# Kernel tuning notes

Hardware: AMD Instinct MI355X
Metric: run time of the kernel (lower is better)

The kernel has to match this reference:

```python
import jax, jax.numpy as jnp
import numpy as np
from functools import partial

EPS = 1e-10


@partial(jax.custom_vjp, nondiff_argnums=(1,))
def kwta(x, k):
    # k-WTA: keep top-k values along last dim, zero elsewhere (STE backward).
    vals, _ = jax.lax.top_k(x, k)
    thresh = vals[..., -1:]
    return jnp.where(x >= thresh, x, jnp.zeros((), x.dtype))


def _kwta_fwd(x, k):
    out = kwta(x, k)
    mask = (out != 0).astype(x.dtype)  # matches torch: mask = (out != 0)
    return out, mask


def _kwta_bwd(k, mask, g):
    return (g * mask,)


kwta.defvjp(_kwta_fwd, _kwta_bwd)


def _sparsify(x, W_down, k):
    h = jax.nn.relu(x @ W_down.T)          # (B, T, N_ca3)
    h = kwta(h, k)
    norm = jnp.maximum(jnp.linalg.norm(h, axis=-1, keepdims=True), EPS)
    return h / norm


def _retrieve_successor(sparse, W_ca3, k):
    # retrieval_steps = 1; replicate the early-break on all-zero activity.
    h = jax.nn.relu(sparse @ W_ca3.T)       # (B, T, N_ca3)
    valid = h.sum() >= EPS
    hk = kwta(h, k)
    norm = jnp.maximum(jnp.linalg.norm(hk, axis=-1, keepdims=True), EPS)
    return jnp.where(valid, hk / norm, sparse)


def setup_inputs() -> dict:
    key = jax.random.key(0)
    k1, k2, k3, k4, k5, k6 = jax.random.split(key, 6)
    B, T, D, N = 4, 2048, 1024, 4096
    x = jax.random.normal(k1, (B, T, D), dtype=jnp.float32)
    # xavier_normal: std = gain * sqrt(2 / (fan_in + fan_out))
    W_down = jax.random.normal(k2, (N, D), dtype=jnp.float32) * (0.5 * np.sqrt(2.0 / (D + N)))
    W_up = jax.random.normal(k3, (D, N), dtype=jnp.float32) * (0.1 * np.sqrt(2.0 / (D + N)))
    # gate_proj weight is zero-init in torch; use small random for a nontrivial gate
    W_gate = jax.random.normal(k4, (D, D), dtype=jnp.float32) * 0.02
    b_gate = jnp.full((D,), -2.0, dtype=jnp.float32)
    # W_ca3 buffer is zero-init then Hebbian-learned; random stand-in
    W_ca3 = jax.random.normal(k6, (N, N), dtype=jnp.float32) * 0.02
    return {"x": x, "W_down": W_down, "W_up": W_up, "W_gate": W_gate,
            "b_gate": b_gate, "W_ca3": W_ca3, "k": 64}


def reference(x, W_down, W_up, W_gate, b_gate, W_ca3, k):
    sparse = _sparsify(x, W_down, k)                    # (B, T, N)
    successor = _retrieve_successor(sparse, W_ca3, k)   # (B, T, N)
    prediction = successor @ W_up.T                     # (B, T, D)
    g = jax.nn.sigmoid(x @ W_gate.T + b_gate)           # (B, T, D)
    return x + g * prediction
```

## Files before the change

### kernel.cpp

```cpp
#include <hip/hip_runtime.h>
#include <hip/hip_bf16.h>
#include <stdint.h>

typedef float f32x4 __attribute__((ext_vector_type(4)));
typedef int i32x4 __attribute__((ext_vector_type(4)));

#define MROWS 8192
#define DD 1024
#define DN 4096

__device__ __forceinline__ void load_lds16(const void* g, void* l) {
  __builtin_amdgcn_global_load_lds((const __attribute__((address_space(1))) void*)g,
                                   (__attribute__((address_space(3))) void*)l, 16, 0, 0);
}

__device__ __forceinline__ unsigned f32_to_bf16_rne(float f) {
  unsigned u = __float_as_uint(f);
  return (u + 0x7fffu + ((u >> 16) & 1u)) >> 16;
}

template<int EPI>
__global__ void __launch_bounds__(512, 1)
gemm_i8_4ph(const uint8_t* __restrict__ A, const uint8_t* __restrict__ B,
            __hip_bfloat16* __restrict__ Cb, int M, int N, int K,
            float* __restrict__ vsum,
            const float* __restrict__ sA, const float* __restrict__ sB)
{
  extern __shared__ __align__(16) char smem[];
  const int tid  = threadIdx.x;
  const int lane = tid & 63;
  const int wave = tid >> 6;
  const int wm = wave >> 2;
  const int wn = wave & 3;

  const int nwg = gridDim.x;
  const int bid = ((int)blockIdx.x % 8) * (nwg >> 3) + ((int)blockIdx.x >> 3);

  const int nbn = N >> 8;
  const int bm = (bid / nbn) << 8;
  const int bn = (bid % nbn) << 8;

  const int NT = K >> 7;

  i32x4 acc[8][4];
  const i32x4 izero = {0, 0, 0, 0};
#pragma unroll
  for (int i = 0; i < 8; ++i)
#pragma unroll
    for (int j = 0; j < 4; ++j)
      acc[i][j] = izero;

  const int csb = (((tid & 3) ^ ((tid >> 3) & 3)) << 4);
  const uint8_t* Ag = A + (size_t)(bm + (tid >> 2)) * K + csb;
  const uint8_t* Bg = B + (size_t)(bn + (tid >> 2)) * K + csb;

  const int rl = lane & 15;
  const int kc = lane >> 4;
  const int chunk_off = ((kc ^ ((rl >> 1) & 3)) << 4);
  const int aoff = ((wm << 7) + rl) * 64 + chunk_off;
  const int boff = ((wn << 6) + rl) * 64 + chunk_off;

#define STAGE_AB(S, KH) do { \
    const int kt_ = (((S) & (NT - 1)) << 7) + ((KH) << 6); \
    char* da_ = smem + (((((S) & 1) << 1) | (KH)) << 14) + (tid << 4); \
    load_lds16(Ag + kt_, da_); \
    load_lds16(Ag + (size_t)128 * K + kt_, da_ + 8192); \
    load_lds16(Bg + kt_, da_ + 65536); \
    load_lds16(Bg + (size_t)128 * K + kt_, da_ + 65536 + 8192); \
  } while (0)

  i32x4 a0, a1, a2, a3, a4, a5, a6, a7, b0, b1, b2, b3;

#define MFMA_ROW8(MI, AF) \
    acc[MI][0] = __builtin_amdgcn_mfma_i32_16x16x64_i8(AF, b0, acc[MI][0], 0, 0, 0); \
    acc[MI][1] = __builtin_amdgcn_mfma_i32_16x16x64_i8(AF, b1, acc[MI][1], 0, 0, 0); \
    acc[MI][2] = __builtin_amdgcn_mfma_i32_16x16x64_i8(AF, b2, acc[MI][2], 0, 0, 0); \
    acc[MI][3] = __builtin_amdgcn_mfma_i32_16x16x64_i8(AF, b3, acc[MI][3], 0, 0, 0);

#define PH4(P, KH, STG) do { \
    { const char* ab_ = smem + ((((P) << 1) | (KH)) << 14) + aoff; \
      a0 = *(const i32x4*)(ab_);        a1 = *(const i32x4*)(ab_ + 1024); \
      a2 = *(const i32x4*)(ab_ + 2048); a3 = *(const i32x4*)(ab_ + 3072); \
      a4 = *(const i32x4*)(ab_ + 4096); a5 = *(const i32x4*)(ab_ + 5120); \
      a6 = *(const i32x4*)(ab_ + 6144); a7 = *(const i32x4*)(ab_ + 7168); \
      const char* bb_ = smem + 65536 + ((((P) << 1) | (KH)) << 14) + boff; \
      b0 = *(const i32x4*)(bb_);        b1 = *(const i32x4*)(bb_ + 1024); \
      b2 = *(const i32x4*)(bb_ + 2048); b3 = *(const i32x4*)(bb_ + 3072); } \
    STG; \
    asm volatile("s_waitcnt vmcnt(8)" ::: "memory"); \
    asm volatile("s_barrier" ::: "memory"); \
    asm volatile("s_waitcnt lgkmcnt(0)" ::: "memory"); \
    __builtin_amdgcn_sched_barrier(0); \
    __builtin_amdgcn_s_setprio(1); \
    MFMA_ROW8(0, a0) MFMA_ROW8(1, a1) MFMA_ROW8(2, a2) MFMA_ROW8(3, a3) \
    MFMA_ROW8(4, a4) MFMA_ROW8(5, a5) MFMA_ROW8(6, a6) MFMA_ROW8(7, a7) \
    __builtin_amdgcn_s_setprio(0); \
    asm volatile("s_barrier" ::: "memory"); \
  } while (0)

  STAGE_AB(0, 0);
  STAGE_AB(0, 1);
  STAGE_AB(1, 0);
  asm volatile("s_waitcnt vmcnt(8)" ::: "memory");
  asm volatile("s_barrier" ::: "memory");

#pragma unroll 1
  for (int t = 0; t < NT; t += 2) {
    PH4(0, 0, STAGE_AB(t + 1, 1));
    PH4(0, 1, STAGE_AB(t + 2, 0));
    PH4(1, 0, STAGE_AB(t + 2, 1));
    PH4(1, 1, STAGE_AB(t + 3, 0));
  }

  const int r0 = bm + (wm << 7) + (kc << 2);
  const int c0 = bn + (wn << 6) + rl;
  float lsum = 0.f;
#pragma unroll
  for (int mi = 0; mi < 8; ++mi) {
#pragma unroll
    for (int nf = 0; nf < 4; ++nf) {
#pragma unroll
      for (int q = 0; q < 4; ++q) {
        const int r = r0 + (mi << 4) + q;
        const int c = c0 + (nf << 4);
        float v = (float)acc[mi][nf][q] * sA[r] * sB[c];
        v = fmaxf(v, 0.f);
        Cb[(size_t)r * N + c] = __float2bfloat16(v);
        if constexpr (EPI == 1) lsum += v;
      }
    }
  }
  if constexpr (EPI == 1) {
#pragma unroll
    for (int off = 32; off > 0; off >>= 1)
      lsum += __shfl_down(lsum, off);
    if (lane == 0) atomicAdd(vsum, lsum);
  }

#undef STAGE_AB
#undef MFMA_ROW8
#undef PH4
}

__global__ void __launch_bounds__(256)
gemm_predgate(const uint8_t* __restrict__ Asp, const uint8_t* __restrict__ Bup,
              const uint8_t* __restrict__ Ax,  const uint8_t* __restrict__ Bg8,
              float* __restrict__ Cf, int M, int N, int K1, int K2,
              const float* __restrict__ sA,  const float* __restrict__ swu,
              const float* __restrict__ sx,  const float* __restrict__ swg,
              const float* __restrict__ Xf,  const float* __restrict__ Bgate)
{
  __shared__ __align__(16) char smem[32768];
  const int tid  = threadIdx.x;
  const int lane = tid & 63;
  const int wave = tid >> 6;

  const int nbn = N >> 7;
  const int bm = ((int)blockIdx.x / nbn) << 7;
  const int bn = ((int)blockIdx.x % nbn) << 7;

  const int wm = (wave >> 1) << 6;
  const int wn = (wave & 1) << 6;

  i32x4 acc1[4][4], acc2[4][4];
  const i32x4 izero = {0, 0, 0, 0};
#pragma unroll
  for (int i = 0; i < 4; ++i)
#pragma unroll
    for (int j = 0; j < 4; ++j) { acc1[i][j] = izero; acc2[i][j] = izero; }

  const int srow = tid >> 3;
  const int schk = (tid & 7) ^ (srow & 7);
  char* ldsA = smem + (wave << 10);
  char* ldsB = smem + 16384 + (wave << 10);

  const int aoff0 = (wm + (lane & 15)) << 7;
  const int boff0 = 16384 + ((wn + (lane & 15)) << 7);
  const int kc = lane >> 4;
  const int sw = lane & 7;

#define K_LOOP(APTR, BPTR, KK, ACC) do { \
    const uint8_t* Ag = (APTR) + (size_t)(bm + srow) * (KK) + (schk << 4); \
    const uint8_t* Bg = (BPTR) + (size_t)(bn + srow) * (KK) + (schk << 4); \
    for (int k0 = 0; k0 < (KK); k0 += 128) { \
      _Pragma("unroll") \
      for (int i = 0; i < 4; ++i) \
        load_lds16(Ag + (size_t)(i << 5) * (KK) + k0, ldsA + (i << 12)); \
      _Pragma("unroll") \
      for (int i = 0; i < 4; ++i) \
        load_lds16(Bg + (size_t)(i << 5) * (KK) + k0, ldsB + (i << 12)); \
      __syncthreads(); \
      _Pragma("unroll") \
      for (int ks = 0; ks < 2; ++ks) { \
        const int cb = ((kc + (ks << 2)) ^ sw) << 4; \
        i32x4 af[4], bfr[4]; \
        _Pragma("unroll") \
        for (int i = 0; i < 4; ++i) \
          af[i] = *reinterpret_cast<const i32x4*>(smem + aoff0 + (i << 11) + cb); \
        _Pragma("unroll") \
        for (int j = 0; j < 4; ++j) \
          bfr[j] = *reinterpret_cast<const i32x4*>(smem + boff0 + (j << 11) + cb); \
        _Pragma("unroll") \
        for (int i = 0; i < 4; ++i) \
          _Pragma("unroll") \
          for (int j = 0; j < 4; ++j) \
            ACC[i][j] = __builtin_amdgcn_mfma_i32_16x16x64_i8(af[i], bfr[j], ACC[i][j], 0, 0, 0); \
      } \
      __syncthreads(); \
    } \
  } while (0)

  K_LOOP(Asp, Bup, K1, acc1);
  K_LOOP(Ax,  Bg8, K2, acc2);
#undef K_LOOP

  const int r0 = bm + wm + ((lane >> 4) << 2);
  const int c0 = bn + wn + (lane & 15);
#pragma unroll
  for (int i = 0; i < 4; ++i) {
#pragma unroll
    for (int j = 0; j < 4; ++j) {
#pragma unroll
      for (int q = 0; q < 4; ++q) {
        const int r = r0 + (i << 4) + q;
        const int c = c0 + (j << 4);
        const size_t idx = (size_t)r * N + c;
        const float pred = (float)acc1[i][j][q] * sA[r] * swu[c];
        const float vg   = (float)acc2[i][j][q] * sx[r] * swg[c] + Bgate[c];
        const float g = 1.f / (1.f + __expf(-vg));
        Cf[idx] = Xf[idx] + g * pred;
      }
    }
  }
}

template<int MODE>
__global__ void __launch_bounds__(256)
kwta_wave(const __hip_bfloat16* __restrict__ H, uint8_t* __restrict__ OUTQ,
          float* __restrict__ sA, const float* __restrict__ vsumPtr,
          const int* __restrict__ kptr)
{
  const int tid  = threadIdx.x;
  const int lane = tid & 63;
  const int w    = tid >> 6;
  const int row  = ((int)blockIdx.x << 2) + w;

  if constexpr (MODE == 1) {
    if (!(*vsumPtr >= 1e-10f)) return;
  }

  const uint4* h8 = (const uint4*)(H + (size_t)row * 4096);
  uint4 d[8];
#pragma unroll
  for (int i = 0; i < 8; ++i) d[i] = h8[(i << 6) + lane];

  const unsigned k = (unsigned)(*kptr);

  unsigned kmax = 0;
#pragma unroll
  for (int i = 0; i < 8; ++i) {
    const unsigned* p = (const unsigned*)&d[i];
#pragma unroll
    for (int c4 = 0; c4 < 4; ++c4) {
      kmax = max(kmax, p[c4] & 0xffffu);
      kmax = max(kmax, p[c4] >> 16);
    }
  }
#pragma unroll
  for (int off = 32; off > 0; off >>= 1) kmax = max(kmax, __shfl_xor(kmax, off));

  unsigned lo = 0, hi = 65536;
#pragma unroll 1
  for (int it = 0; it < 16; ++it) {
    const unsigned mid = (lo + hi) >> 1;
    unsigned c = 0;
#pragma unroll
    for (int i = 0; i < 8; ++i) {
      const unsigned* p = (const unsigned*)&d[i];
#pragma unroll
      for (int c4 = 0; c4 < 4; ++c4) {
        c += ((p[c4] & 0xffffu) >= mid) ? 1u : 0u;
        c += ((p[c4] >> 16) >= mid) ? 1u : 0u;
      }
    }
#pragma unroll
    for (int off = 32; off > 0; off >>= 1) c += __shfl_xor(c, off);
    if (c >= k) lo = mid; else hi = mid;
  }
  const unsigned threshKey = lo;

  float ss = 0.f;
#pragma unroll
  for (int i = 0; i < 8; ++i) {
    const unsigned* p = (const unsigned*)&d[i];
#pragma unroll
    for (int c4 = 0; c4 < 4; ++c4) {
#pragma unroll
      for (int hh = 0; hh < 2; ++hh) {
        const unsigned key = hh ? (p[c4] >> 16) : (p[c4] & 0xffffu);
        if (key >= threshKey) {
          const float v = __uint_as_float(key << 16);
          ss = fmaf(v, v, ss);
        }
      }
    }
  }
#pragma unroll
  for (int off = 32; off > 0; off >>= 1) ss += __shfl_xor(ss, off);
  const float inv = 1.f / fmaxf(sqrtf(ss), 1e-10f);

  const float vmaxf = __uint_as_float(kmax << 16);
  const float r127 = (kmax > 0) ? 127.f / vmaxf : 0.f;

  if (lane == 0) sA[row] = vmaxf * inv * (1.f / 127.f);

  uint2* o2 = (uint2*)(OUTQ + (size_t)row * 4096);
#pragma unroll
  for (int i = 0; i < 8; ++i) {
    const unsigned* p = (const unsigned*)&d[i];
    unsigned b[8];
#pragma unroll
    for (int c4 = 0; c4 < 4; ++c4) {
#pragma unroll
      for (int hh = 0; hh < 2; ++hh) {
        const unsigned key = hh ? (p[c4] >> 16) : (p[c4] & 0xffffu);
        unsigned q = 0;
        if (key >= threshKey && key > 0) {
          const float v = __uint_as_float(key << 16);
          q = (unsigned)__float2int_rn(v * r127) & 0xffu;
        }
        b[c4 * 2 + hh] = q;
      }
    }
    uint2 o;
    o.x = b[0] | (b[1] << 8) | (b[2] << 16) | (b[3] << 24);
    o.y = b[4] | (b[5] << 8) | (b[6] << 16) | (b[7] << 24);
    o2[(i << 6) + lane] = o;
  }
}

__global__ void __launch_bounds__(256)
quant1024(const float* __restrict__ X, const float* __restrict__ Wd,
          const float* __restrict__ Wg,
          uint8_t* __restrict__ xq, uint8_t* __restrict__ wdq,
          uint8_t* __restrict__ wgq,
          float* __restrict__ sx, float* __restrict__ swd,
          float* __restrict__ swg)
{
  const int wgl = ((int)blockIdx.x << 2) + (threadIdx.x >> 6);
  const int lane = threadIdx.x & 63;

  const float* W; uint8_t* q; float* s; int row;
  if      (wgl < 8192)  { W = X;  q = xq;  s = sx;  row = wgl; }
  else if (wgl < 12288) { W = Wd; q = wdq; s = swd; row = wgl - 8192; }
  else                  { W = Wg; q = wgq; s = swg; row = wgl - 12288; }

  const float4* src = (const float4*)(W + (size_t)row * 1024);
  float4 v[4];
  float am = 0.f;
#pragma unroll
  for (int i = 0; i < 4; ++i) {
    v[i] = src[(i << 6) + lane];
    am = fmaxf(am, fmaxf(fmaxf(fabsf(v[i].x), fabsf(v[i].y)),
                         fmaxf(fabsf(v[i].z), fabsf(v[i].w))));
  }
#pragma unroll
  for (int off = 32; off > 0; off >>= 1) am = fmaxf(am, __shfl_xor(am, off));

  const float rinv = (am > 0.f) ? 127.f / am : 0.f;
  uint4 o;
  unsigned* ob = (unsigned*)&o;
#pragma unroll
  for (int i = 0; i < 4; ++i) {
    const unsigned b0 = (unsigned)__float2int_rn(v[i].x * rinv) & 0xffu;
    const unsigned b1 = (unsigned)__float2int_rn(v[i].y * rinv) & 0xffu;
    const unsigned b2 = (unsigned)__float2int_rn(v[i].z * rinv) & 0xffu;
    const unsigned b3 = (unsigned)__float2int_rn(v[i].w * rinv) & 0xffu;
    ob[i] = b0 | (b1 << 8) | (b2 << 16) | (b3 << 24);
  }
  ((uint4*)(q + (size_t)row * 1024))[lane] = o;
  if (lane == 0) s[row] = am * (1.f / 127.f);
}

__global__ void __launch_bounds__(256)
quant4096(const float* __restrict__ Wc, const float* __restrict__ Wu,
          uint8_t* __restrict__ qc, uint8_t* __restrict__ qu,
          float* __restrict__ sc, float* __restrict__ su)
{
  const int wgl = ((int)blockIdx.x << 2) + (threadIdx.x >> 6);
  const int lane = threadIdx.x & 63;

  const float* W; uint8_t* q; float* s; int row;
  if (wgl < 4096) { W = Wc; q = qc; s = sc; row = wgl; }
  else            { W = Wu; q = qu; s = su; row = wgl - 4096; }

  const float4* src = (const float4*)(W + (size_t)row * 4096);
  float4 v[16];
  float am = 0.f;
#pragma unroll
  for (int i = 0; i < 16; ++i) {
    v[i] = src[(i << 6) + lane];
    am = fmaxf(am, fmaxf(fmaxf(fabsf(v[i].x), fabsf(v[i].y)),
                         fmaxf(fabsf(v[i].z), fabsf(v[i].w))));
  }
#pragma unroll
  for (int off = 32; off > 0; off >>= 1) am = fmaxf(am, __shfl_xor(am, off));

  const float rinv = (am > 0.f) ? 127.f / am : 0.f;
  unsigned* qo = (unsigned*)(q + (size_t)row * 4096);
#pragma unroll
  for (int i = 0; i < 16; ++i) {
    const unsigned b0 = (unsigned)__float2int_rn(v[i].x * rinv) & 0xffu;
    const unsigned b1 = (unsigned)__float2int_rn(v[i].y * rinv) & 0xffu;
    const unsigned b2 = (unsigned)__float2int_rn(v[i].z * rinv) & 0xffu;
    const unsigned b3 = (unsigned)__float2int_rn(v[i].w * rinv) & 0xffu;
    qo[(i << 6) + lane] = b0 | (b1 << 8) | (b2 << 16) | (b3 << 24);
  }
  if (lane == 0) s[row] = am * (1.f / 127.f);
}

__global__ void diag_kernel(float* out, float mb)
{
  if (threadIdx.x == 0 && blockIdx.x == 0) out[0] = -mb;
}

extern "C" void kernel_launch(void* const* d_in, const int* in_sizes, int n_in,
                              void* d_out, int out_size, void* d_ws, size_t ws_size,
                              hipStream_t stream)
{
  const float* x     = (const float*)d_in[0];
  const float* Wdown = (const float*)d_in[1];
  const float* Wup   = (const float*)d_in[2];
  const float* Wgate = (const float*)d_in[3];
  const float* bgate = (const float*)d_in[4];
  const float* Wca3  = (const float*)d_in[5];
  const int*   kptr  = (const int*)d_in[6];

  const size_t OFF_XQ   = 0;
  const size_t OFF_WDQ  = 8388608;
  const size_t OFF_WGQ  = 12582912;
  const size_t OFF_WCQ  = 13631488;
  const size_t OFF_WUQ  = 30408704;
  const size_t OFF_SX   = 34603008;
  const size_t OFF_SWD  = 34635776;
  const size_t OFF_SWG  = 34652160;
  const size_t OFF_SWC  = 34656256;
  const size_t OFF_SWU  = 34672640;
  const size_t OFF_SA   = 34676736;
  const size_t OFF_VSUM = 34709504;
  const size_t OFF_SPQ  = 34713600;
  const size_t OFF_H    = 68268032;
  const size_t NEED     = 135376896;

  if (ws_size < NEED) {
    diag_kernel<<<1, 64, 0, stream>>>((float*)d_out, (float)(ws_size >> 20));
    return;
  }

  char* ws = (char*)d_ws;
  uint8_t*        xq   = (uint8_t*)       (ws + OFF_XQ);
  uint8_t*        wdq  = (uint8_t*)       (ws + OFF_WDQ);
  uint8_t*        wgq  = (uint8_t*)       (ws + OFF_WGQ);
  uint8_t*        wcq  = (uint8_t*)       (ws + OFF_WCQ);
  uint8_t*        wuq  = (uint8_t*)       (ws + OFF_WUQ);
  float*          sx   = (float*)         (ws + OFF_SX);
  float*          swd  = (float*)         (ws + OFF_SWD);
  float*          swg  = (float*)         (ws + OFF_SWG);
  float*          swc  = (float*)         (ws + OFF_SWC);
  float*          swu  = (float*)         (ws + OFF_SWU);
  float*          sA   = (float*)         (ws + OFF_SA);
  float*          vsum = (float*)         (ws + OFF_VSUM);
  uint8_t*        spq  = (uint8_t*)       (ws + OFF_SPQ);
  __hip_bfloat16* h    = (__hip_bfloat16*)(ws + OFF_H);

  hipMemsetAsync(vsum, 0, sizeof(float), stream);

  quant1024<<<3328, 256, 0, stream>>>(x, Wdown, Wgate, xq, wdq, wgq, sx, swd, swg);
  quant4096<<<1280, 256, 0, stream>>>(Wca3, Wup, wcq, wuq, swc, swu);

  gemm_i8_4ph<0><<<(MROWS >> 8) * (DN >> 8), 512, 131072, stream>>>(
      xq, wdq, h, MROWS, DN, DD, nullptr, sx, swd);
  kwta_wave<0><<<MROWS / 4, 256, 0, stream>>>(h, spq, sA, nullptr, kptr);
  gemm_i8_4ph<1><<<(MROWS >> 8) * (DN >> 8), 512, 131072, stream>>>(
      spq, wcq, h, MROWS, DN, DN, vsum, sA, swc);
  kwta_wave<1><<<MROWS / 4, 256, 0, stream>>>(h, spq, sA, vsum, kptr);
  gemm_predgate<<<(MROWS >> 7) * (DD >> 7), 256, 0, stream>>>(
      spq, wuq, xq, wgq, (float*)d_out, MROWS, DD, DN, DD,
      sA, swu, sx, swg, x, bgate);
}
```

Baseline: 465.0 us.

## Replace dense CA3 and up-projection GEMMs with sparse top-k gathers

The k-WTA output is now stored as compacted (index, value) lists capped per row, instead of a dense int8 matrix. The 4096x4096 CA3 GEMM and the up-projection GEMM become gathers over transposed int8 weight rows, which exploits the roughly 64-of-4096 sparsity. The gate GEMM is split into its own kernel that writes bf16 logits, the first GEMM is re-pipelined into eight finer phases, and a transpose kernel is added. In exchange it adds a per-call weight transpose and a fixed cap that could truncate rows with many ties at the threshold.

```diff
diff --git a/kernel.cpp b/kernel.cpp
--- a/kernel.cpp
+++ b/kernel.cpp
@@ -8,6 +8,7 @@
 #define MROWS 8192
 #define DD 1024
 #define DN 4096
+#define CAP 160
 
 __device__ __forceinline__ void load_lds16(const void* g, void* l) {
   __builtin_amdgcn_global_load_lds((const __attribute__((address_space(1))) void*)g,
@@ -19,11 +20,9 @@
   return (u + 0x7fffu + ((u >> 16) & 1u)) >> 16;
 }
 
-template<int EPI>
 __global__ void __launch_bounds__(512, 1)
-gemm_i8_4ph(const uint8_t* __restrict__ A, const uint8_t* __restrict__ B,
+gemm_i8_8ph(const uint8_t* __restrict__ A, const uint8_t* __restrict__ B,
             __hip_bfloat16* __restrict__ Cb, int M, int N, int K,
-            float* __restrict__ vsum,
             const float* __restrict__ sA, const float* __restrict__ sB)
 {
   extern __shared__ __align__(16) char smem[];
@@ -60,16 +59,22 @@
   const int aoff = ((wm << 7) + rl) * 64 + chunk_off;
   const int boff = ((wn << 6) + rl) * 64 + chunk_off;
 
-#define STAGE_AB(S, KH) do { \
+#define STAGE_A8(S, KH) do { \
     const int kt_ = (((S) & (NT - 1)) << 7) + ((KH) << 6); \
-    char* da_ = smem + (((((S) & 1) << 1) | (KH)) << 14) + (tid << 4); \
-    load_lds16(Ag + kt_, da_); \
-    load_lds16(Ag + (size_t)128 * K + kt_, da_ + 8192); \
-    load_lds16(Bg + kt_, da_ + 65536); \
-    load_lds16(Bg + (size_t)128 * K + kt_, da_ + 65536 + 8192); \
+    char* dst_ = smem + (((((S) & 1) << 1) | (KH)) << 14) + (tid << 4); \
+    load_lds16(Ag + kt_, dst_); \
+    load_lds16(Ag + (size_t)128 * K + kt_, dst_ + 8192); \
   } while (0)
 
-  i32x4 a0, a1, a2, a3, a4, a5, a6, a7, b0, b1, b2, b3;
+#define STAGE_B8(S, KH) do { \
+    const int kt_ = (((S) & (NT - 1)) << 7) + ((KH) << 6); \
+    char* dst_ = smem + 65536 + (((((S) & 1) << 1) | (KH)) << 14) + (tid << 4); \
+    load_lds16(Bg + kt_, dst_); \
+    load_lds16(Bg + (size_t)128 * K + kt_, dst_ + 8192); \
+  } while (0)
+
+  i32x4 afS[2][4];
+  i32x4 b0, b1, b2, b3;
 
 #define MFMA_ROW8(MI, AF) \
     acc[MI][0] = __builtin_amdgcn_mfma_i32_16x16x64_i8(AF, b0, acc[MI][0], 0, 0, 0); \
@@ -77,44 +82,59 @@
     acc[MI][2] = __builtin_amdgcn_mfma_i32_16x16x64_i8(AF, b2, acc[MI][2], 0, 0, 0); \
     acc[MI][3] = __builtin_amdgcn_mfma_i32_16x16x64_i8(AF, b3, acc[MI][3], 0, 0, 0);
 
-#define PH4(P, KH, STG) do { \
-    { const char* ab_ = smem + ((((P) << 1) | (KH)) << 14) + aoff; \
-      a0 = *(const i32x4*)(ab_);        a1 = *(const i32x4*)(ab_ + 1024); \
-      a2 = *(const i32x4*)(ab_ + 2048); a3 = *(const i32x4*)(ab_ + 3072); \
-      a4 = *(const i32x4*)(ab_ + 4096); a5 = *(const i32x4*)(ab_ + 5120); \
-      a6 = *(const i32x4*)(ab_ + 6144); a7 = *(const i32x4*)(ab_ + 7168); \
-      const char* bb_ = smem + 65536 + ((((P) << 1) | (KH)) << 14) + boff; \
-      b0 = *(const i32x4*)(bb_);        b1 = *(const i32x4*)(bb_ + 1024); \
-      b2 = *(const i32x4*)(bb_ + 2048); b3 = *(const i32x4*)(bb_ + 3072); } \
+#define PH8(PN, KHN, MHN, ASETN, ACUR, MHC, DOBP, BP, BKH, STG, VM) do { \
+    { const char* ab_ = smem + ((((PN) << 1) | (KHN)) << 14) + aoff + (MHN) * 4096; \
+      afS[ASETN][0] = *(const i32x4*)(ab_); \
+      afS[ASETN][1] = *(const i32x4*)(ab_ + 1024); \
+      afS[ASETN][2] = *(const i32x4*)(ab_ + 2048); \
+      afS[ASETN][3] = *(const i32x4*)(ab_ + 3072); } \
     STG; \
-    asm volatile("s_waitcnt vmcnt(8)" ::: "memory"); \
+    if (VM) { asm volatile("s_waitcnt vmcnt(6)" ::: "memory"); } \
     asm volatile("s_barrier" ::: "memory"); \
-    asm volatile("s_waitcnt lgkmcnt(0)" ::: "memory"); \
     __builtin_amdgcn_sched_barrier(0); \
     __builtin_amdgcn_s_setprio(1); \
-    MFMA_ROW8(0, a0) MFMA_ROW8(1, a1) MFMA_ROW8(2, a2) MFMA_ROW8(3, a3) \
-    MFMA_ROW8(4, a4) MFMA_ROW8(5, a5) MFMA_ROW8(6, a6) MFMA_ROW8(7, a7) \
+    MFMA_ROW8((MHC) * 4 + 0, afS[ACUR][0]) \
+    MFMA_ROW8((MHC) * 4 + 1, afS[ACUR][1]) \
+    MFMA_ROW8((MHC) * 4 + 2, afS[ACUR][2]) \
+    MFMA_ROW8((MHC) * 4 + 3, afS[ACUR][3]) \
     __builtin_amdgcn_s_setprio(0); \
+    if (DOBP) { \
+      const char* bb_ = smem + 65536 + ((((BP) << 1) | (BKH)) << 14) + boff; \
+      b0 = *(const i32x4*)(bb_); b1 = *(const i32x4*)(bb_ + 1024); \
+      b2 = *(const i32x4*)(bb_ + 2048); b3 = *(const i32x4*)(bb_ + 3072); } \
     asm volatile("s_barrier" ::: "memory"); \
   } while (0)
 
-  STAGE_AB(0, 0);
-  STAGE_AB(0, 1);
-  STAGE_AB(1, 0);
-  asm volatile("s_waitcnt vmcnt(8)" ::: "memory");
+  STAGE_A8(0, 0); STAGE_B8(0, 0);
+  STAGE_A8(0, 1); STAGE_B8(0, 1);
+  STAGE_A8(1, 0); STAGE_B8(1, 0);
+  asm volatile("s_waitcnt vmcnt(4)" ::: "memory");
   asm volatile("s_barrier" ::: "memory");
+  {
+    const char* ab_ = smem + aoff;
+    afS[1][0] = *(const i32x4*)(ab_);
+    afS[1][1] = *(const i32x4*)(ab_ + 1024);
+    afS[1][2] = *(const i32x4*)(ab_ + 2048);
+    afS[1][3] = *(const i32x4*)(ab_ + 3072);
+    const char* bb_ = smem + 65536 + boff;
+    b0 = *(const i32x4*)(bb_); b1 = *(const i32x4*)(bb_ + 1024);
+    b2 = *(const i32x4*)(bb_ + 2048); b3 = *(const i32x4*)(bb_ + 3072);
+  }
 
 #pragma unroll 1
   for (int t = 0; t < NT; t += 2) {
-    PH4(0, 0, STAGE_AB(t + 1, 1));
-    PH4(0, 1, STAGE_AB(t + 2, 0));
-    PH4(1, 0, STAGE_AB(t + 2, 1));
-    PH4(1, 1, STAGE_AB(t + 3, 0));
+    PH8(0, 0, 1, 0, 1, 0, 0, 0, 0, STAGE_A8(t + 1, 1), 1);
+    PH8(0, 1, 0, 1, 0, 1, 1, 0, 1, STAGE_B8(t + 1, 1), 0);
+    PH8(0, 1, 1, 0, 1, 0, 0, 0, 0, STAGE_A8(t + 2, 0), 1);
+    PH8(1, 0, 0, 1, 0, 1, 1, 1, 0, STAGE_B8(t + 2, 0), 0);
+    PH8(1, 0, 1, 0, 1, 0, 0, 0, 0, STAGE_A8(t + 2, 1), 1);
+    PH8(1, 1, 0, 1, 0, 1, 1, 1, 1, STAGE_B8(t + 2, 1), 0);
+    PH8(1, 1, 1, 0, 1, 0, 0, 0, 0, STAGE_A8(t + 3, 0), 1);
+    PH8(0, 0, 0, 1, 0, 1, 1, 0, 0, STAGE_B8(t + 3, 0), 0);
   }
 
   const int r0 = bm + (wm << 7) + (kc << 2);
   const int c0 = bn + (wn << 6) + rl;
-  float lsum = 0.f;
 #pragma unroll
   for (int mi = 0; mi < 8; ++mi) {
 #pragma unroll
@@ -124,31 +144,21 @@
         const int r = r0 + (mi << 4) + q;
         const int c = c0 + (nf << 4);
         float v = (float)acc[mi][nf][q] * sA[r] * sB[c];
-        v = fmaxf(v, 0.f);
-        Cb[(size_t)r * N + c] = __float2bfloat16(v);
-        if constexpr (EPI == 1) lsum += v;
+        Cb[(size_t)r * N + c] = __float2bfloat16(fmaxf(v, 0.f));
       }
     }
   }
-  if constexpr (EPI == 1) {
-#pragma unroll
-    for (int off = 32; off > 0; off >>= 1)
-      lsum += __shfl_down(lsum, off);
-    if (lane == 0) atomicAdd(vsum, lsum);
-  }
-
-#undef STAGE_AB
+
+#undef STAGE_A8
+#undef STAGE_B8
 #undef MFMA_ROW8
-#undef PH4
+#undef PH8
 }
 
 __global__ void __launch_bounds__(256)
-gemm_predgate(const uint8_t* __restrict__ Asp, const uint8_t* __restrict__ Bup,
-              const uint8_t* __restrict__ Ax,  const uint8_t* __restrict__ Bg8,
-              float* __restrict__ Cf, int M, int N, int K1, int K2,
-              const float* __restrict__ sA,  const float* __restrict__ swu,
-              const float* __restrict__ sx,  const float* __restrict__ swg,
-              const float* __restrict__ Xf,  const float* __restrict__ Bgate)
+gemm_gate_i8(const uint8_t* __restrict__ A, const uint8_t* __restrict__ B,
+             __hip_bfloat16* __restrict__ Cb, int M, int N, int K,
+             const float* __restrict__ sA, const float* __restrict__ sB)
 {
   __shared__ __align__(16) char smem[32768];
   const int tid  = threadIdx.x;
@@ -162,15 +172,17 @@
   const int wm = (wave >> 1) << 6;
   const int wn = (wave & 1) << 6;
 
-  i32x4 acc1[4][4], acc2[4][4];
+  i32x4 acc[4][4];
   const i32x4 izero = {0, 0, 0, 0};
 #pragma unroll
   for (int i = 0; i < 4; ++i)
 #pragma unroll
-    for (int j = 0; j < 4; ++j) { acc1[i][j] = izero; acc2[i][j] = izero; }
+    for (int j = 0; j < 4; ++j) acc[i][j] = izero;
 
   const int srow = tid >> 3;
   const int schk = (tid & 7) ^ (srow & 7);
+  const uint8_t* Ag = A + (size_t)(bm + srow) * K + (schk << 4);
+  const uint8_t* Bg = B + (size_t)(bn + srow) * K + (schk << 4);
   char* ldsA = smem + (wave << 10);
   char* ldsB = smem + 16384 + (wave << 10);
 
@@ -179,95 +191,64 @@
   const int kc = lane >> 4;
   const int sw = lane & 7;
 
-#define K_LOOP(APTR, BPTR, KK, ACC) do { \
-    const uint8_t* Ag = (APTR) + (size_t)(bm + srow) * (KK) + (schk << 4); \
-    const uint8_t* Bg = (BPTR) + (size_t)(bn + srow) * (KK) + (schk << 4); \
-    for (int k0 = 0; k0 < (KK); k0 += 128) { \
-      _Pragma("unroll") \
-      for (int i = 0; i < 4; ++i) \
-        load_lds16(Ag + (size_t)(i << 5) * (KK) + k0, ldsA + (i << 12)); \
-      _Pragma("unroll") \
-      for (int i = 0; i < 4; ++i) \
-        load_lds16(Bg + (size_t)(i << 5) * (KK) + k0, ldsB + (i << 12)); \
-      __syncthreads(); \
-      _Pragma("unroll") \
-      for (int ks = 0; ks < 2; ++ks) { \
-        const int cb = ((kc + (ks << 2)) ^ sw) << 4; \
-        i32x4 af[4], bfr[4]; \
-        _Pragma("unroll") \
-        for (int i = 0; i < 4; ++i) \
-          af[i] = *reinterpret_cast<const i32x4*>(smem + aoff0 + (i << 11) + cb); \
-        _Pragma("unroll") \
-        for (int j = 0; j < 4; ++j) \
-          bfr[j] = *reinterpret_cast<const i32x4*>(smem + boff0 + (j << 11) + cb); \
-        _Pragma("unroll") \
-        for (int i = 0; i < 4; ++i) \
-          _Pragma("unroll") \
-          for (int j = 0; j < 4; ++j) \
-            ACC[i][j] = __builtin_amdgcn_mfma_i32_16x16x64_i8(af[i], bfr[j], ACC[i][j], 0, 0, 0); \
-      } \
-      __syncthreads(); \
-    } \
-  } while (0)
-
-  K_LOOP(Asp, Bup, K1, acc1);
-  K_LOOP(Ax,  Bg8, K2, acc2);
-#undef K_LOOP
+  for (int k0 = 0; k0 < K; k0 += 128) {
+#pragma unroll
+    for (int i = 0; i < 4; ++i)
+      load_lds16(Ag + (size_t)(i << 5) * K + k0, ldsA + (i << 12));
+#pragma unroll
+    for (int i = 0; i < 4; ++i)
+      load_lds16(Bg + (size_t)(i << 5) * K + k0, ldsB + (i << 12));
+    __syncthreads();
+#pragma unroll
+    for (int ks = 0; ks < 2; ++ks) {
+      const int cb = ((kc + (ks << 2)) ^ sw) << 4;
+      i32x4 af[4], bfr[4];
+#pragma unroll
+      for (int i = 0; i < 4; ++i)
+        af[i] = *reinterpret_cast<const i32x4*>(smem + aoff0 + (i << 11) + cb);
+#pragma unroll
+      for (int j = 0; j < 4; ++j)
+        bfr[j] = *reinterpret_cast<const i32x4*>(smem + boff0 + (j << 11) + cb);
+#pragma unroll
+      for (int i = 0; i < 4; ++i)
+#pragma unroll
+        for (int j = 0; j < 4; ++j)
+          acc[i][j] = __builtin_amdgcn_mfma_i32_16x16x64_i8(af[i], bfr[j], acc[i][j], 0, 0, 0);
+    }
+    __syncthreads();
+  }
 
   const int r0 = bm + wm + ((lane >> 4) << 2);
   const int c0 = bn + wn + (lane & 15);
 #pragma unroll
-  for (int i = 0; i < 4; ++i) {
-#pragma unroll
-    for (int j = 0; j < 4; ++j) {
+  for (int i = 0; i < 4; ++i)
+#pragma unroll
+    for (int j = 0; j < 4; ++j)
 #pragma unroll
       for (int q = 0; q < 4; ++q) {
         const int r = r0 + (i << 4) + q;
         const int c = c0 + (j << 4);
-        const size_t idx = (size_t)r * N + c;
-        const float pred = (float)acc1[i][j][q] * sA[r] * swu[c];
-        const float vg   = (float)acc2[i][j][q] * sx[r] * swg[c] + Bgate[c];
-        const float g = 1.f / (1.f + __expf(-vg));
-        Cf[idx] = Xf[idx] + g * pred;
+        Cb[(size_t)r * N + c] =
+            __float2bfloat16((float)acc[i][j][q] * sA[r] * sB[c]);
       }
-    }
-  }
-}
-
-template<int MODE>
+}
+
 __global__ void __launch_bounds__(256)
-kwta_wave(const __hip_bfloat16* __restrict__ H, uint8_t* __restrict__ OUTQ,
-          float* __restrict__ sA, const float* __restrict__ vsumPtr,
-          const int* __restrict__ kptr)
+kwta_compact(const __hip_bfloat16* __restrict__ H,
+             unsigned short* __restrict__ sp_idx, float* __restrict__ sp_val,
+             unsigned* __restrict__ sp_cnt, const int* __restrict__ kptr)
 {
   const int tid  = threadIdx.x;
   const int lane = tid & 63;
   const int w    = tid >> 6;
   const int row  = ((int)blockIdx.x << 2) + w;
 
-  if constexpr (MODE == 1) {
-    if (!(*vsumPtr >= 1e-10f)) return;
-  }
-
   const uint4* h8 = (const uint4*)(H + (size_t)row * 4096);
   uint4 d[8];
 #pragma unroll
   for (int i = 0; i < 8; ++i) d[i] = h8[(i << 6) + lane];
 
   const unsigned k = (unsigned)(*kptr);
-
-  unsigned kmax = 0;
-#pragma unroll
-  for (int i = 0; i < 8; ++i) {
-    const unsigned* p = (const unsigned*)&d[i];
-#pragma unroll
-    for (int c4 = 0; c4 < 4; ++c4) {
-      kmax = max(kmax, p[c4] & 0xffffu);
-      kmax = max(kmax, p[c4] >> 16);
-    }
-  }
-#pragma unroll
-  for (int off = 32; off > 0; off >>= 1) kmax = max(kmax, __shfl_xor(kmax, off));
 
   unsigned lo = 0, hi = 65536;
 #pragma unroll 1
@@ -287,9 +268,10 @@
     for (int off = 32; off > 0; off >>= 1) c += __shfl_xor(c, off);
     if (c >= k) lo = mid; else hi = mid;
   }
-  const unsigned threshKey = lo;
+  const unsigned T = lo;
 
   float ss = 0.f;
+  unsigned kc = 0;
 #pragma unroll
   for (int i = 0; i < 8; ++i) {
     const unsigned* p = (const unsigned*)&d[i];
@@ -298,9 +280,10 @@
 #pragma unroll
       for (int hh = 0; hh < 2; ++hh) {
         const unsigned key = hh ? (p[c4] >> 16) : (p[c4] & 0xffffu);
-        if (key >= threshKey) {
+        if (key >= T && key > 0) {
           const float v = __uint_as_float(key << 16);
           ss = fmaf(v, v, ss);
+          ++kc;
         }
       }
     }
@@ -309,33 +292,228 @@
   for (int off = 32; off > 0; off >>= 1) ss += __shfl_xor(ss, off);
   const float inv = 1.f / fmaxf(sqrtf(ss), 1e-10f);
 
-  const float vmaxf = __uint_as_float(kmax << 16);
-  const float r127 = (kmax > 0) ? 127.f / vmaxf : 0.f;
-
-  if (lane == 0) sA[row] = vmaxf * inv * (1.f / 127.f);
-
-  uint2* o2 = (uint2*)(OUTQ + (size_t)row * 4096);
+  unsigned inc = kc;
+#pragma unroll
+  for (int off = 1; off < 64; off <<= 1) {
+    const unsigned n = __shfl_up(inc, off);
+    if (lane >= off) inc += n;
+  }
+  unsigned pos = inc - kc;
+  const unsigned total = __shfl(inc, 63);
+
+  const size_t base = (size_t)row * CAP;
 #pragma unroll
   for (int i = 0; i < 8; ++i) {
     const unsigned* p = (const unsigned*)&d[i];
-    unsigned b[8];
 #pragma unroll
     for (int c4 = 0; c4 < 4; ++c4) {
 #pragma unroll
       for (int hh = 0; hh < 2; ++hh) {
         const unsigned key = hh ? (p[c4] >> 16) : (p[c4] & 0xffffu);
-        unsigned q = 0;
-        if (key >= threshKey && key > 0) {
-          const float v = __uint_as_float(key << 16);
-          q = (unsigned)__float2int_rn(v * r127) & 0xffu;
+        if (key >= T && key > 0) {
+          if (pos < CAP) {
+            sp_idx[base + pos] = (unsigned short)((((i << 6) + lane) << 3) + c4 * 2 + hh);
+            sp_val[base + pos] = __uint_as_float(key << 16) * inv;
+          }
+          ++pos;
         }
-        b[c4 * 2 + hh] = q;
       }
     }
-    uint2 o;
-    o.x = b[0] | (b[1] << 8) | (b[2] << 16) | (b[3] << 24);
-    o.y = b[4] | (b[5] << 8) | (b[6] << 16) | (b[7] << 24);
-    o2[(i << 6) + lane] = o;
+  }
+  if (lane == 0) sp_cnt[row] = total < CAP ? total : CAP;
+}
+
+__global__ void __launch_bounds__(256)
+ca3_gather(const unsigned short* __restrict__ sp_idx, const float* __restrict__ sp_val,
+           const unsigned* __restrict__ sp_cnt,
+           const uint8_t* __restrict__ wct, const float* __restrict__ swc,
+           unsigned short* __restrict__ succ_idx, float* __restrict__ succ_val,
+           unsigned* __restrict__ succ_cnt,
+           float* __restrict__ vsum, const int* __restrict__ kptr)
+{
+  __shared__ float redf[4];
+  __shared__ unsigned redu[8];
+
+  const int row  = blockIdx.x;
+  const int tid  = threadIdx.x;
+  const int lane = tid & 63;
+  const int w    = tid >> 6;
+  const int cb   = tid << 4;
+
+  const int cnt = (int)sp_cnt[row];
+  const unsigned short* ji = sp_idx + (size_t)row * CAP;
+  const float* vi = sp_val + (size_t)row * CAP;
+
+  float acc[16];
+#pragma unroll
+  for (int e = 0; e < 16; ++e) acc[e] = 0.f;
+  float vsumc = 0.f;
+
+  uint4 wcur = {0, 0, 0, 0};
+  float v0 = 0.f;
+  if (cnt > 0) {
+    const int j0 = ji[0];
+    v0 = vi[0];
+    wcur = *(const uint4*)(wct + (size_t)j0 * 4096 + cb);
+  }
+#pragma unroll 1
+  for (int i = 0; i < cnt; ++i) {
+    uint4 wn = {0, 0, 0, 0};
+    float vn = 0.f;
+    if (i + 1 < cnt) {
+      const int jn = ji[i + 1];
+      vn = vi[i + 1];
+      wn = *(const uint4*)(wct + (size_t)jn * 4096 + cb);
+    }
+    const float v = v0;
+    vsumc += v;
+#define UNP(word, b_) \
+    acc[b_ + 0] = fmaf(v, (float)((word) & 0xffu), acc[b_ + 0]); \
+    acc[b_ + 1] = fmaf(v, (float)(((word) >> 8) & 0xffu), acc[b_ + 1]); \
+    acc[b_ + 2] = fmaf(v, (float)(((word) >> 16) & 0xffu), acc[b_ + 2]); \
+    acc[b_ + 3] = fmaf(v, (float)((word) >> 24), acc[b_ + 3]);
+    UNP(wcur.x, 0) UNP(wcur.y, 4) UNP(wcur.z, 8) UNP(wcur.w, 12)
+#undef UNP
+    wcur = wn; v0 = vn;
+  }
+
+  const float corr = 128.f * vsumc;
+  float vals[16];
+  unsigned keys[16];
+  float rs = 0.f;
+#pragma unroll
+  for (int e = 0; e < 16; ++e) {
+    const float h = fmaxf((acc[e] - corr) * swc[cb + e], 0.f);
+    const unsigned kk = f32_to_bf16_rne(h);
+    keys[e] = kk;
+    vals[e] = __uint_as_float(kk << 16);
+    rs += vals[e];
+  }
+
+#pragma unroll
+  for (int off = 32; off > 0; off >>= 1) rs += __shfl_xor(rs, off);
+  if (lane == 0) redf[w] = rs;
+  __syncthreads();
+  if (tid == 0) atomicAdd(vsum, redf[0] + redf[1] + redf[2] + redf[3]);
+
+  const unsigned k = (unsigned)(*kptr);
+  unsigned lo = 0, hi = 65536;
+#pragma unroll 1
+  for (int it = 0; it < 16; ++it) {
+    const unsigned mid = (lo + hi) >> 1;
+    unsigned c = 0;
+#pragma unroll
+    for (int e = 0; e < 16; ++e) c += (keys[e] >= mid) ? 1u : 0u;
+#pragma unroll
+    for (int off = 32; off > 0; off >>= 1) c += __shfl_xor(c, off);
+    if (lane == 0) redu[w] = c;
+    __syncthreads();
+    const unsigned tot = redu[0] + redu[1] + redu[2] + redu[3];
+    if (tot >= k) lo = mid; else hi = mid;
+    __syncthreads();
+  }
+  const unsigned T = lo;
+
+  float ss = 0.f;
+  unsigned kc = 0;
+#pragma unroll
+  for (int e = 0; e < 16; ++e) {
+    if (keys[e] >= T && keys[e] > 0) {
+      ss = fmaf(vals[e], vals[e], ss);
+      ++kc;
+    }
+  }
+#pragma unroll
+  for (int off = 32; off > 0; off >>= 1) ss += __shfl_xor(ss, off);
+  if (lane == 0) redf[w] = ss;
+  __syncthreads();
+  const float inv = 1.f / fmaxf(sqrtf(redf[0] + redf[1] + redf[2] + redf[3]), 1e-10f);
+
+  unsigned inc = kc;
+#pragma unroll
+  for (int off = 1; off < 64; off <<= 1) {
+    const unsigned n = __shfl_up(inc, off);
+    if (lane >= off) inc += n;
+  }
+  if (lane == 63) redu[4 + w] = inc;
+  __syncthreads();
+  unsigned wbase = 0;
+#pragma unroll
+  for (int ww = 0; ww < 4; ++ww)
+    if (ww < w) wbase += redu[4 + ww];
+  unsigned pos = wbase + inc - kc;
+  const unsigned total = redu[4] + redu[5] + redu[6] + redu[7];
+
+  const size_t base = (size_t)row * CAP;
+#pragma unroll
+  for (int e = 0; e < 16; ++e) {
+    if (keys[e] >= T && keys[e] > 0) {
+      if (pos < CAP) {
+        succ_idx[base + pos] = (unsigned short)(cb + e);
+        succ_val[base + pos] = vals[e] * inv;
+      }
+      ++pos;
+    }
+  }
+  if (tid == 0) succ_cnt[row] = total < CAP ? total : CAP;
+}
+
+__global__ void __launch_bounds__(256)
+final_gather(const unsigned short* __restrict__ sp_idx, const float* __restrict__ sp_val,
+             const unsigned* __restrict__ sp_cnt,
+             const unsigned short* __restrict__ succ_idx, const float* __restrict__ succ_val,
+             const unsigned* __restrict__ succ_cnt,
+             const float* __restrict__ vsum,
+             const uint8_t* __restrict__ wut, const float* __restrict__ swu,
+             const __hip_bfloat16* __restrict__ glin, const float* __restrict__ bg,
+             const float* __restrict__ x, float* __restrict__ out)
+{
+  const int row = blockIdx.x;
+  const int tid = threadIdx.x;
+  const int cb  = tid << 2;
+
+  const bool valid = (*vsum >= 1e-10f);
+  const unsigned short* ji = (valid ? succ_idx : sp_idx) + (size_t)row * CAP;
+  const float* vi = (valid ? succ_val : sp_val) + (size_t)row * CAP;
+  const int cnt = (int)((valid ? succ_cnt : sp_cnt)[row]);
+
+  float acc[4] = {0.f, 0.f, 0.f, 0.f};
+  float vs = 0.f;
+
+  unsigned wcur = 0;
+  float v0 = 0.f;
+  if (cnt > 0) {
+    const int j0 = ji[0];
+    v0 = vi[0];
+    wcur = *(const unsigned*)(wut + (size_t)j0 * 1024 + cb);
+  }
+#pragma unroll 1
+  for (int i = 0; i < cnt; ++i) {
+    unsigned wn = 0;
+    float vn = 0.f;
+    if (i + 1 < cnt) {
+      const int jn = ji[i + 1];
+      vn = vi[i + 1];
+      wn = *(const unsigned*)(wut + (size_t)jn * 1024 + cb);
+    }
+    const float v = v0;
+    vs += v;
+    acc[0] = fmaf(v, (float)(wcur & 0xffu), acc[0]);
+    acc[1] = fmaf(v, (float)((wcur >> 8) & 0xffu), acc[1]);
+    acc[2] = fmaf(v, (float)((wcur >> 16) & 0xffu), acc[2]);
+    acc[3] = fmaf(v, (float)(wcur >> 24), acc[3]);
+    wcur = wn; v0 = vn;
+  }
+
+  const float corr = 128.f * vs;
+  const size_t rbase = (size_t)row * 1024;
+#pragma unroll
+  for (int e = 0; e < 4; ++e) {
+    const int c = cb + e;
+    const float pred = (acc[e] - corr) * swu[c];
+    const float gl = __bfloat162float(glin[rbase + c]) + bg[c];
+    const float g = 1.f / (1.f + __expf(-gl));
+    out[rbase + c] = x[rbase + c] + g * pred;
   }
 }
 
@@ -419,6 +597,41 @@
   if (lane == 0) s[row] = am * (1.f / 127.f);
 }
 
+__global__ void __launch_bounds__(256)
+transpose_i8(const uint8_t* __restrict__ wcq, uint8_t* __restrict__ wct,
+             const uint8_t* __restrict__ wuq, uint8_t* __restrict__ wut)
+{
+  __shared__ char tile[64][68];
+  int b = blockIdx.x;
+  const uint8_t* src; uint8_t* dst; int c0, j0, Kd;
+  if (b < 4096) { src = wcq; dst = wct; c0 = (b >> 6) << 6; j0 = (b & 63) << 6; Kd = 4096; }
+  else { b -= 4096; src = wuq; dst = wut; c0 = (b >> 6) << 6; j0 = (b & 63) << 6; Kd = 1024; }
+
+  const int t = threadIdx.x;
+  const int r = t >> 2;
+  const int ch = t & 3;
+
+  const uint4 v = *(const uint4*)(src + (size_t)(c0 + r) * 4096 + j0 + (ch << 4));
+  *(unsigned*)&tile[r][(ch << 4) + 0]  = v.x;
+  *(unsigned*)&tile[r][(ch << 4) + 4]  = v.y;
+  *(unsigned*)&tile[r][(ch << 4) + 8]  = v.z;
+  *(unsigned*)&tile[r][(ch << 4) + 12] = v.w;
+  __syncthreads();
+
+  uint4 o;
+  unsigned* ow = (unsigned*)&o;
+#pragma unroll
+  for (int qw = 0; qw < 4; ++qw) {
+    const int ccb = (ch << 4) + (qw << 2);
+    const unsigned b0 = (unsigned)(unsigned char)tile[ccb + 0][r];
+    const unsigned b1 = (unsigned)(unsigned char)tile[ccb + 1][r];
+    const unsigned b2 = (unsigned)(unsigned char)tile[ccb + 2][r];
+    const unsigned b3 = (unsigned)(unsigned char)tile[ccb + 3][r];
+    ow[qw] = (b0 | (b1 << 8) | (b2 << 16) | (b3 << 24)) ^ 0x80808080u;
+  }
+  *(uint4*)(dst + (size_t)(j0 + r) * Kd + c0 + (ch << 4)) = o;
+}
+
 __global__ void diag_kernel(float* out, float mb)
 {
   if (threadIdx.x == 0 && blockIdx.x == 0) out[0] = -mb;
@@ -441,16 +654,23 @@
   const size_t OFF_WGQ  = 12582912;
   const size_t OFF_WCQ  = 13631488;
   const size_t OFF_WUQ  = 30408704;
-  const size_t OFF_SX   = 34603008;
-  const size_t OFF_SWD  = 34635776;
-  const size_t OFF_SWG  = 34652160;
-  const size_t OFF_SWC  = 34656256;
-  const size_t OFF_SWU  = 34672640;
-  const size_t OFF_SA   = 34676736;
-  const size_t OFF_VSUM = 34709504;
-  const size_t OFF_SPQ  = 34713600;
-  const size_t OFF_H    = 68268032;
-  const size_t NEED     = 135376896;
+  const size_t OFF_WCT  = 34603008;
+  const size_t OFF_WUT  = 51380224;
+  const size_t OFF_SX   = 55574528;
+  const size_t OFF_SWD  = 55607296;
+  const size_t OFF_SWG  = 55623680;
+  const size_t OFF_SWC  = 55627776;
+  const size_t OFF_SWU  = 55644160;
+  const size_t OFF_VSUM = 55648256;
+  const size_t OFF_SPI  = 55652352;
+  const size_t OFF_SPV  = 58273792;
+  const size_t OFF_SPC  = 63516672;
+  const size_t OFF_SUI  = 63549440;
+  const size_t OFF_SUV  = 66170880;
+  const size_t OFF_SUC  = 71413760;
+  const size_t OFF_GL   = 71446528;
+  const size_t OFF_H    = 88223744;
+  const size_t NEED     = 155332608;
 
   if (ws_size < NEED) {
     diag_kernel<<<1, 64, 0, stream>>>((float*)d_out, (float)(ws_size >> 20));
@@ -458,33 +678,41 @@
   }
 
   char* ws = (char*)d_ws;
-  uint8_t*        xq   = (uint8_t*)       (ws + OFF_XQ);
-  uint8_t*        wdq  = (uint8_t*)       (ws + OFF_WDQ);
-  uint8_t*        wgq  = (uint8_t*)       (ws + OFF_WGQ);
-  uint8_t*        wcq  = (uint8_t*)       (ws + OFF_WCQ);
-  uint8_t*        wuq  = (uint8_t*)       (ws + OFF_WUQ);
-  float*          sx   = (float*)         (ws + OFF_SX);
-  float*          swd  = (float*)         (ws + OFF_SWD);
-  float*          swg  = (float*)         (ws + OFF_SWG);
-  float*          swc  = (float*)         (ws + OFF_SWC);
-  float*          swu  = (float*)         (ws + OFF_SWU);
-  float*          sA   = (float*)         (ws + OFF_SA);
-  float*          vsum = (float*)         (ws + OFF_VSUM);
-  uint8_t*        spq  = (uint8_t*)       (ws + OFF_SPQ);
+  uint8_t*        xq   = (uint8_t*)(ws + OFF_XQ);
+  uint8_t*        wdq  = (uint8_t*)(ws + OFF_WDQ);
+  uint8_t*        wgq  = (uint8_t*)(ws + OFF_WGQ);
+  uint8_t*        wcq  = (uint8_t*)(ws + OFF_WCQ);
+  uint8_t*        wuq  = (uint8_t*)(ws + OFF_WUQ);
+  uint8_t*        wct  = (uint8_t*)(ws + OFF_WCT);
+  uint8_t*        wut  = (uint8_t*)(ws + OFF_WUT);
+  float*          sx   = (float*)(ws + OFF_SX);
+  float*          swd  = (float*)(ws + OFF_SWD);
+  float*          swg  = (float*)(ws + OFF_SWG);
+  float*          swc  = (float*)(ws + OFF_SWC);
+  float*          swu  = (float*)(ws + OFF_SWU);
+  float*          vsum = (float*)(ws + OFF_VSUM);
+  unsigned short* spi  = (unsigned short*)(ws + OFF_SPI);
+  float*          spv  = (float*)(ws + OFF_SPV);
+  unsigned*       spc  = (unsigned*)(ws + OFF_SPC);
+  unsigned short* sui  = (unsigned short*)(ws + OFF_SUI);
+  float*          suv  = (float*)(ws + OFF_SUV);
+  unsigned*       suc  = (unsigned*)(ws + OFF_SUC);
+  __hip_bfloat16* gl   = (__hip_bfloat16*)(ws + OFF_GL);
   __hip_bfloat16* h    = (__hip_bfloat16*)(ws + OFF_H);
 
   hipMemsetAsync(vsum, 0, sizeof(float), stream);
 
   quant1024<<<3328, 256, 0, stream>>>(x, Wdown, Wgate, xq, wdq, wgq, sx, swd, swg);
   quant4096<<<1280, 256, 0, stream>>>(Wca3, Wup, wcq, wuq, swc, swu);
-
-  gemm_i8_4ph<0><<<(MROWS >> 8) * (DN >> 8), 512, 131072, stream>>>(
-      xq, wdq, h, MROWS, DN, DD, nullptr, sx, swd);
-  kwta_wave<0><<<MROWS / 4, 256, 0, stream>>>(h, spq, sA, nullptr, kptr);
-  gemm_i8_4ph<1><<<(MROWS >> 8) * (DN >> 8), 512, 131072, stream>>>(
-      spq, wcq, h, MROWS, DN, DN, vsum, sA, swc);
-  kwta_wave<1><<<MROWS / 4, 256, 0, stream>>>(h, spq, sA, vsum, kptr);
-  gemm_predgate<<<(MROWS >> 7) * (DD >> 7), 256, 0, stream>>>(
-      spq, wuq, xq, wgq, (float*)d_out, MROWS, DD, DN, DD,
-      sA, swu, sx, swg, x, bgate);
-}
+  transpose_i8<<<5120, 256, 0, stream>>>(wcq, wct, wuq, wut);
+
+  gemm_i8_8ph<<<(MROWS >> 8) * (DN >> 8), 512, 131072, stream>>>(
+      xq, wdq, h, MROWS, DN, DD, sx, swd);
+  kwta_compact<<<MROWS / 4, 256, 0, stream>>>(h, spi, spv, spc, kptr);
+  gemm_gate_i8<<<(MROWS >> 7) * (DD >> 7), 256, 0, stream>>>(
+      xq, wgq, gl, MROWS, DD, DD, sx, swg);
+  ca3_gather<<<MROWS, 256, 0, stream>>>(spi, spv, spc, wct, swc,
+                                        sui, suv, suc, vsum, kptr);
+  final_gather<<<MROWS, 256, 0, stream>>>(spi, spv, spc, sui, suv, suc, vsum,
+                                          wut, swu, gl, bgate, x, (float*)d_out);
+}
```

Result: slower. 559.3 us (+20.3%).
